# Kernel optimization log

Measured on AMD Instinct MI355X. Metric: run time of the kernel, lower is better.

Reference implementation:

```python
import jax, jax.numpy as jnp
import numpy as np

R = 15  # receptive-field rows (self.rfield)
_NAMES = ['1x', '2x', '3x', '4x', '1e', '2e', '3e', '4e', '5', '6', '7', '8', '9']
_CIN = [3, 64, 64, 64, 3, 64, 64, 64, 64, 64, 64, 64, 64]
_COUT = [64, 64, 64, 64, 64, 64, 64, 64, 64, 64, 64, 64, 3]


def _leaky(x):
    return jnp.where(x >= 0, x, 0.01 * x)  # nn.LeakyReLU default slope


def _conv(x, w, b, ph):
    # 3x3 conv, stride 1, padding (ph, 1) matching torch Conv2d padding=[ph, 1]
    y = jax.lax.conv_general_dilated(x, w, (1, 1), ((ph, ph), (1, 1)),
                                     dimension_numbers=('NCHW', 'OIHW', 'NCHW'))
    return y + b[None, :, None, None]


def setup_inputs():
    key = jax.random.key(0)
    ks = jax.random.split(key, len(_NAMES) + 1)
    inp = {'x': jax.random.normal(ks[0], (1, 3, 31, 256), jnp.float32)}
    for j, n in enumerate(_NAMES):
        std = np.float32((2.0 / (_CIN[j] * 9)) ** 0.5)  # He init for 3x3 conv
        inp['w' + n] = jax.random.normal(ks[j + 1], (_COUT[j], _CIN[j], 3, 3), jnp.float32) * std
        inp['b' + n] = jnp.zeros((_COUT[j],), jnp.float32)
    return inp


def _predict(s, e, p):
    # x-branch: 15 rows -> 9 rows (three H-valid convs)
    for n, ph in (('1x', 1), ('2x', 0), ('3x', 0), ('4x', 0)):
        s = _leaky(_conv(s, p['w' + n], p['b' + n], ph))
    # e-branch
    for n, ph in (('1e', 1), ('2e', 0), ('3e', 0), ('4e', 0)):
        e = _leaky(_conv(e, p['w' + n], p['b' + n], ph))
    B, C, Hs, W = s.shape  # C == 64 -> per-pixel 8x8 matrices; Hs == R - 6 == 9
    sr = jnp.transpose(s, (0, 2, 3, 1)).reshape(B, Hs, W, 8, 8)
    er = jnp.transpose(e, (0, 2, 3, 1)).reshape(B, Hs, W, 8, 8)
    pr = jnp.einsum('bhwij,bhwjk->bhwik', er, sr).reshape(B, Hs, W, 64)
    pr = jnp.transpose(pr, (0, 3, 1, 2))  # [B,64,9,W]
    # fuse stack: 9 rows -> 1 row, then 64 -> 3 channels
    for n, ph in (('5', 0), ('6', 0), ('7', 0), ('8', 0), ('9', 1)):
        pr = _leaky(_conv(pr, p['w' + n], p['b' + n], ph))
    return pr  # [B, 3, 1, W]


def _forward(x, p):
    B, C, H, W = x.shape

    def step(ebuf, i):
        # torch code sets error = x (alias), so slice_x and slice_e are the SAME mutated buffer
        sl = jax.lax.dynamic_slice(ebuf, (0, 0, i, 0), (B, C, R, W))
        pr = _predict(sl, sl, p)
        # act_row reads row ky of the (mutated) x, but row ky is overwritten only after this read,
        # so it still equals the original input row
        act = jax.lax.dynamic_slice(x, (0, 0, i + R, 0), (B, C, 1, W))
        ebuf = jax.lax.dynamic_update_slice(ebuf, act - pr, (0, 0, i + R, 0))
        return ebuf, pr

    ebuf, preds = jax.lax.scan(step, x, jnp.arange(H - R))
    pred = jnp.transpose(preds[:, :, :, 0, :], (1, 2, 0, 3))  # [S,B,C,1,W] -> [B,C,S,W]
    # 'truth' is read from the in-place-mutated x, i.e. the residual buffer, matching the torch aliasing bug/behavior
    truth = ebuf[:, :, R:, :]
    return pred, truth


def reference(x, w1x, b1x, w2x, b2x, w3x, b3x, w4x, b4x, w1e, b1e, w2e, b2e, w3e, b3e, w4e, b4e, w5, b5, w6, b6, w7, b7, w8, b8, w9, b9):
    p = dict(w1x=w1x, b1x=b1x, w2x=w2x, b2x=b2x, w3x=w3x, b3x=b3x, w4x=w4x, b4x=b4x,
             w1e=w1e, b1e=b1e, w2e=w2e, b2e=b2e, w3e=w3e, b3e=b3e, w4e=w4e, b4e=b4e,
             w5=w5, b5=b5, w6=w6, b6=b6, w7=w7, b7=b7, w8=w8, b8=b8, w9=w9, b9=b9)
    return _forward(x, p)
```

## Files before the change

### kernel.cpp

```cpp
#include <hip/hip_runtime.h>

#define LEAKY(v) ((v) >= 0.f ? (v) : 0.01f * (v))

__global__ __launch_bounds__(256, 2) void conv3Q(
    const float* __restrict__ ebuf, int i0,
    const float* __restrict__ w0, const float* __restrict__ b0,
    const float* __restrict__ w1, const float* __restrict__ b1,
    float* __restrict__ out)
{
    const int lane = threadIdx.x & 63;
    const int wv   = threadIdx.x >> 6;
    const int h  = blockIdx.y;
    const int cq = blockIdx.z & 3;
    const int z  = blockIdx.z >> 2;
    const int cout0 = __builtin_amdgcn_readfirstlane(cq * 16 + wv * 4);
    const float* W  = (z ? w1 : w0) + cout0 * 27;
    const float* Bv = z ? b1 : b0;

    float a[4][4] = {};
    #pragma unroll
    for (int kh = 0; kh < 3; ++kh) {
        const int r = h - 1 + kh;
        const bool valid = (r >= 0 && r < 15);
        const float msk = valid ? 1.f : 0.f;
        #pragma unroll
        for (int c = 0; c < 3; ++c) {
            const float* rr = ebuf + c * (31 * 256) + (i0 + (valid ? r : 0)) * 256 + lane * 4;
            float4 v = *(const float4*)rr;
            v.x *= msk; v.y *= msk; v.z *= msk; v.w *= msk;
            float wl = __shfl_up(v.w, 1);   if (lane == 0)  wl = 0.f;
            float wr = __shfl_down(v.x, 1); if (lane == 63) wr = 0.f;
            const float win[6] = {wl, v.x, v.y, v.z, v.w, wr};
            #pragma unroll
            for (int j = 0; j < 4; ++j) {
                const float* wj = W + j * 27 + c * 9 + kh * 3;
                #pragma unroll
                for (int cc = 0; cc < 4; ++cc)
                    a[j][cc] += wj[0] * win[cc] + wj[1] * win[cc + 1] + wj[2] * win[cc + 2];
            }
        }
    }
    float* o = out + (size_t)z * 245760 + h * 256 + lane * 4;
    #pragma unroll
    for (int j = 0; j < 4; ++j) {
        const float bb = Bv[cout0 + j];
        float4 r4;
        r4.x = LEAKY(a[j][0] + bb);
        r4.y = LEAKY(a[j][1] + bb);
        r4.z = LEAKY(a[j][2] + bb);
        r4.w = LEAKY(a[j][3] + bb);
        *(float4*)(o + (cout0 + j) * (15 * 256)) = r4;
    }
}

template<int HOUT, int INH, int NZ>
__global__ __launch_bounds__(256, 2) void convYQ(
    const float* __restrict__ in,
    const float* __restrict__ w0, const float* __restrict__ b0,
    const float* __restrict__ w1, const float* __restrict__ b1,
    float* __restrict__ out)
{
    const int lane = threadIdx.x;
    const int y    = threadIdx.y;
    const int h  = blockIdx.y;
    const int gz = blockIdx.z;
    const int z    = (NZ == 2) ? (gz >> 6) : 0;
    const int cout = (NZ == 2) ? (gz & 63) : gz;
    const float* W  = (z ? w1 : w0) + cout * 576 + y * 16 * 9;
    const float* Bv = z ? b1 : b0;
    const float* ib = in + (size_t)z * (64 * INH * 256)
                         + y * 16 * (INH * 256) + h * 256 + lane * 4;

    float acc[4] = {};

    #pragma unroll 4
    for (int c = 0; c < 16; ++c) {
        const float* r_ = ib + c * (INH * 256);
        #pragma unroll
        for (int kh = 0; kh < 3; ++kh) {
            float4 v = *(const float4*)(r_ + kh * 256);
            float wl = __shfl_up(v.w, 1);   if (lane == 0)  wl = 0.f;
            float wr = __shfl_down(v.x, 1); if (lane == 63) wr = 0.f;
            const float win[6] = {wl, v.x, v.y, v.z, v.w, wr};
            const float* wj = W + c * 9 + kh * 3;
            #pragma unroll
            for (int cc = 0; cc < 4; ++cc)
                acc[cc] += wj[0] * win[cc] + wj[1] * win[cc + 1] + wj[2] * win[cc + 2];
        }
    }

    __shared__ float red[4][256];
    *(float4*)&red[y][lane * 4] = *(float4*)acc;
    __syncthreads();

    const int col = y * 64 + lane;
    float v = Bv[cout] + red[0][col] + red[1][col] + red[2][col] + red[3][col];
    float* o = out + (size_t)z * (64 * HOUT * 256) + cout * (HOUT * 256) + h * 256;
    o[col] = LEAKY(v);
}

__global__ __launch_bounds__(256, 2) void mm88(const float* __restrict__ tw,
                                               float* __restrict__ p0)
{
    const int idx = blockIdx.x * 256 + threadIdx.x;
    const int i   = blockIdx.y;
    const float* s = tw;
    const float* e = tw + 64 * 9 * 256;
    float sv[64];
    #pragma unroll
    for (int c = 0; c < 64; ++c) sv[c] = s[c * (9 * 256) + idx];
    float ev[8];
    #pragma unroll
    for (int j = 0; j < 8; ++j) ev[j] = e[(i * 8 + j) * (9 * 256) + idx];
    #pragma unroll
    for (int k = 0; k < 8; ++k) {
        float acc = 0.f;
        #pragma unroll
        for (int j = 0; j < 8; ++j) acc += ev[j] * sv[j * 8 + k];
        p0[(i * 8 + k) * (9 * 256) + idx] = acc;
    }
}

__global__ void conv9up(const float* __restrict__ pin, const float* __restrict__ w9,
                        const float* __restrict__ b9, const float* __restrict__ x,
                        float* __restrict__ ebuf, float* __restrict__ preds, int i)
{
    const int wcol = threadIdx.x;
    const int yq   = threadIdx.y;
    const int c0   = yq * 16;
    const bool mL = (wcol > 0), mR = (wcol < 255);
    float a0 = 0.f, a1 = 0.f, a2 = 0.f;

    #pragma unroll 4
    for (int c = 0; c < 16; ++c) {
        const int cin = c0 + c;
        const float* r_ = pin + cin * 256;
        float vm = mL ? r_[wcol - 1] : 0.f;
        float v0 = r_[wcol];
        float vp = mR ? r_[wcol + 1] : 0.f;
        const float* wk0 = w9 + (0 * 64 + cin) * 9 + 3;
        const float* wk1 = w9 + (1 * 64 + cin) * 9 + 3;
        const float* wk2 = w9 + (2 * 64 + cin) * 9 + 3;
        a0 += vm * wk0[0] + v0 * wk0[1] + vp * wk0[2];
        a1 += vm * wk1[0] + v0 * wk1[1] + vp * wk1[2];
        a2 += vm * wk2[0] + v0 * wk2[1] + vp * wk2[2];
    }

    __shared__ float red[4][3][256];
    red[yq][0][wcol] = a0;
    red[yq][1][wcol] = a1;
    red[yq][2][wcol] = a2;
    __syncthreads();

    if (yq == 0) {
        #pragma unroll
        for (int j = 0; j < 3; ++j) {
            float v = b9[j] + red[0][j][wcol] + red[1][j][wcol]
                            + red[2][j][wcol] + red[3][j][wcol];
            v = LEAKY(v);
            preds[i * 768 + j * 256 + wcol] = v;
            ebuf[j * 31 * 256 + (15 + i) * 256 + wcol] =
                x[j * 31 * 256 + (15 + i) * 256 + wcol] - v;
        }
    }
}

__global__ void finalize(const float* __restrict__ preds, const float* __restrict__ ebuf,
                         float* __restrict__ o)
{
    const int idx = blockIdx.x * 256 + threadIdx.x;
    if (idx >= 24576) return;
    if (idx < 12288) {
        const int c = idx >> 12;
        const int t = (idx >> 8) & 15;
        const int w = idx & 255;
        o[idx] = preds[t * 768 + c * 256 + w];
    } else {
        const int j = idx - 12288;
        const int c = j >> 12;
        const int t = (j >> 8) & 15;
        const int w = j & 255;
        o[idx] = ebuf[c * 31 * 256 + (15 + t) * 256 + w];
    }
}

extern "C" void kernel_launch(void* const* d_in, const int* in_sizes, int n_in,
                              void* d_out, int out_size, void* d_ws, size_t ws_size,
                              hipStream_t stream)
{
    const float* x   = (const float*)d_in[0];
    const float* w1x = (const float*)d_in[1];  const float* b1x = (const float*)d_in[2];
    const float* w2x = (const float*)d_in[3];  const float* b2x = (const float*)d_in[4];
    const float* w3x = (const float*)d_in[5];  const float* b3x = (const float*)d_in[6];
    const float* w4x = (const float*)d_in[7];  const float* b4x = (const float*)d_in[8];
    const float* w1e = (const float*)d_in[9];  const float* b1e = (const float*)d_in[10];
    const float* w2e = (const float*)d_in[11]; const float* b2e = (const float*)d_in[12];
    const float* w3e = (const float*)d_in[13]; const float* b3e = (const float*)d_in[14];
    const float* w4e = (const float*)d_in[15]; const float* b4e = (const float*)d_in[16];
    const float* w5  = (const float*)d_in[17]; const float* b5  = (const float*)d_in[18];
    const float* w6  = (const float*)d_in[19]; const float* b6  = (const float*)d_in[20];
    const float* w7  = (const float*)d_in[21]; const float* b7  = (const float*)d_in[22];
    const float* w8  = (const float*)d_in[23]; const float* b8  = (const float*)d_in[24];
    const float* w9  = (const float*)d_in[25]; const float* b9  = (const float*)d_in[26];

    float* ws    = (float*)d_ws;
    float* ebuf  = ws;
    float* tA    = ebuf + 23808;
    float* tB    = tA + 491520;
    float* p0    = tB + 491520;
    float* p1    = p0 + 147456;
    float* preds = p1 + 147456;

    hipMemcpyAsync(ebuf, x, 23808 * sizeof(float), hipMemcpyDeviceToDevice, stream);

    const dim3 cb(64, 4);
    for (int i = 0; i < 16; ++i) {
        conv3Q<<<dim3(1, 15, 8), 256, 0, stream>>>(ebuf, i, w1x, b1x, w1e, b1e, tA);
        convYQ<13, 15, 2><<<dim3(1, 13, 128), cb, 0, stream>>>(tA, w2x, b2x, w2e, b2e, tB);
        convYQ<11, 13, 2><<<dim3(1, 11, 128), cb, 0, stream>>>(tB, w3x, b3x, w3e, b3e, tA);
        convYQ<9, 11, 2><<<dim3(1, 9, 128), cb, 0, stream>>>(tA, w4x, b4x, w4e, b4e, tB);
        mm88<<<dim3(9, 8), 256, 0, stream>>>(tB, p0);
        convYQ<7, 9, 1><<<dim3(1, 7, 64), cb, 0, stream>>>(p0, w5, b5, w5, b5, p1);
        convYQ<5, 7, 1><<<dim3(1, 5, 64), cb, 0, stream>>>(p1, w6, b6, w6, b6, p0);
        convYQ<3, 5, 1><<<dim3(1, 3, 64), cb, 0, stream>>>(p0, w7, b7, w7, b7, p1);
        convYQ<1, 3, 1><<<dim3(1, 1, 64), cb, 0, stream>>>(p1, w8, b8, w8, b8, p0);
        conv9up<<<dim3(1, 1, 1), dim3(256, 4), 0, stream>>>(p0, w9, b9, x, ebuf, preds, i);
    }

    finalize<<<96, 256, 0, stream>>>(preds, ebuf, (float*)d_out);
}
```

Before: 1.919 ms.

## Recompute only changed rows per scan step using ring-buffered layer activations

Per-layer activations now live in ring buffers, with separate slots for the padded top and bottom rows. After the first full pass, each step recomputes only the rows that depend on the newly written error row or the shifted window, instead of redoing every layer over all rows. This removes most of the redundant conv work across the 16 sequential steps. In exchange the slot indexing is intricate and easy to get wrong, and each step still issues a similar number of small kernel launches.

```diff
diff --git a/kernel.cpp b/kernel.cpp
--- a/kernel.cpp
+++ b/kernel.cpp
@@ -2,10 +2,109 @@
 
 #define LEAKY(v) ((v) >= 0.f ? (v) : 0.01f * (v))
 
-__global__ __launch_bounds__(256, 2) void conv3Q(
-    const float* __restrict__ ebuf, int i0,
-    const float* __restrict__ w0, const float* __restrict__ b0,
-    const float* __restrict__ w1, const float* __restrict__ b1,
+#define CS   4608
+#define ZS1  294912
+#define TSL  16
+#define BSL  17
+#define EBCS 7936
+
+struct JobD { const float* t0; const float* t1; const float* t2; float* o; };
+struct IncP { JobD jd[6]; };
+
+__global__ __launch_bounds__(256, 2) void convInc(
+    IncP P, const float* __restrict__ W0, const float* __restrict__ B0,
+    const float* __restrict__ W1, const float* __restrict__ B1,
+    int zsel, int ics, int ocs)
+{
+    const int lane = threadIdx.x;
+    const int y    = threadIdx.y;
+    const int q    = blockIdx.x >> 6;
+    const int cout = blockIdx.x & 63;
+    const int z    = (zsel >> q) & 1;
+    const float* W  = (z ? W1 : W0) + cout * 576 + y * 144;
+    const float* Bv = z ? B1 : B0;
+    const JobD jd  = P.jd[q];
+    const int yo   = y * 16 * ics + lane * 4;
+    const float* t0 = jd.t0 + yo;
+    const float* t1 = jd.t1 + yo;
+    const float* t2 = jd.t2 + yo;
+
+    float acc[4] = {};
+    #pragma unroll 4
+    for (int c = 0; c < 16; ++c) {
+        #pragma unroll
+        for (int t = 0; t < 3; ++t) {
+            const float* rp = (t == 0 ? t0 : (t == 1 ? t1 : t2)) + c * ics;
+            float4 v = *(const float4*)rp;
+            float wl = __shfl_up(v.w, 1);   if (lane == 0)  wl = 0.f;
+            float wr = __shfl_down(v.x, 1); if (lane == 63) wr = 0.f;
+            const float win[6] = {wl, v.x, v.y, v.z, v.w, wr};
+            const float* wj = W + c * 9 + t * 3;
+            #pragma unroll
+            for (int cc = 0; cc < 4; ++cc)
+                acc[cc] += wj[0] * win[cc] + wj[1] * win[cc + 1] + wj[2] * win[cc + 2];
+        }
+    }
+
+    __shared__ float red[4][256];
+    *(float4*)&red[y][lane * 4] = *(float4*)acc;
+    __syncthreads();
+    const int col = y * 64 + lane;
+    float v = Bv[cout] + red[0][col] + red[1][col] + red[2][col] + red[3][col];
+    jd.o[cout * ocs + col] = LEAKY(v);
+}
+
+struct C3P { const float* t[3][3]; float* o[3][2]; };
+
+__global__ __launch_bounds__(256, 2) void conv3inc(
+    C3P P, const float* __restrict__ W0, const float* __restrict__ B0,
+    const float* __restrict__ W1, const float* __restrict__ B1)
+{
+    const int lane = threadIdx.x & 63;
+    const int wv   = threadIdx.x >> 6;
+    const int job  = blockIdx.x >> 3;
+    const int cq   = blockIdx.x & 3;
+    const int z    = (blockIdx.x >> 2) & 1;
+    const int cout0 = __builtin_amdgcn_readfirstlane(cq * 16 + wv * 4);
+    const float* W  = (z ? W1 : W0) + cout0 * 27;
+    const float* Bv = z ? B1 : B0;
+
+    float a[4][4] = {};
+    #pragma unroll
+    for (int t = 0; t < 3; ++t) {
+        const float* rp = P.t[job][t];
+        if (rp) {
+            #pragma unroll
+            for (int c = 0; c < 3; ++c) {
+                float4 v = *(const float4*)(rp + c * EBCS + lane * 4);
+                float wl = __shfl_up(v.w, 1);   if (lane == 0)  wl = 0.f;
+                float wr = __shfl_down(v.x, 1); if (lane == 63) wr = 0.f;
+                const float win[6] = {wl, v.x, v.y, v.z, v.w, wr};
+                #pragma unroll
+                for (int j = 0; j < 4; ++j) {
+                    const float* wj = W + j * 27 + c * 9 + t * 3;
+                    #pragma unroll
+                    for (int cc = 0; cc < 4; ++cc)
+                        a[j][cc] += wj[0] * win[cc] + wj[1] * win[cc + 1] + wj[2] * win[cc + 2];
+                }
+            }
+        }
+    }
+    float* o = P.o[job][z];
+    #pragma unroll
+    for (int j = 0; j < 4; ++j) {
+        const float bb = Bv[cout0 + j];
+        float4 r4;
+        r4.x = LEAKY(a[j][0] + bb); r4.y = LEAKY(a[j][1] + bb);
+        r4.z = LEAKY(a[j][2] + bb); r4.w = LEAKY(a[j][3] + bb);
+        *(float4*)(o + (cout0 + j) * CS + lane * 4) = r4;
+    }
+}
+
+__global__ __launch_bounds__(256, 2) void conv3B(
+    const float* __restrict__ ebuf,
+    const float* __restrict__ W0, const float* __restrict__ B0,
+    const float* __restrict__ W1, const float* __restrict__ B1,
     float* __restrict__ out)
 {
     const int lane = threadIdx.x & 63;
@@ -14,8 +113,8 @@
     const int cq = blockIdx.z & 3;
     const int z  = blockIdx.z >> 2;
     const int cout0 = __builtin_amdgcn_readfirstlane(cq * 16 + wv * 4);
-    const float* W  = (z ? w1 : w0) + cout0 * 27;
-    const float* Bv = z ? b1 : b0;
+    const float* W  = (z ? W1 : W0) + cout0 * 27;
+    const float* Bv = z ? B1 : B0;
 
     float a[4][4] = {};
     #pragma unroll
@@ -25,7 +124,7 @@
         const float msk = valid ? 1.f : 0.f;
         #pragma unroll
         for (int c = 0; c < 3; ++c) {
-            const float* rr = ebuf + c * (31 * 256) + (i0 + (valid ? r : 0)) * 256 + lane * 4;
+            const float* rr = ebuf + c * EBCS + (valid ? r : 0) * 256 + lane * 4;
             float4 v = *(const float4*)rr;
             v.x *= msk; v.y *= msk; v.z *= msk; v.w *= msk;
             float wl = __shfl_up(v.w, 1);   if (lane == 0)  wl = 0.f;
@@ -40,24 +139,23 @@
             }
         }
     }
-    float* o = out + (size_t)z * 245760 + h * 256 + lane * 4;
+    const int slot = (h == 0) ? TSL : (h == 14 ? BSL : (h & 15));
+    float* o = out + (size_t)z * ZS1 + slot * 256;
     #pragma unroll
     for (int j = 0; j < 4; ++j) {
         const float bb = Bv[cout0 + j];
         float4 r4;
-        r4.x = LEAKY(a[j][0] + bb);
-        r4.y = LEAKY(a[j][1] + bb);
-        r4.z = LEAKY(a[j][2] + bb);
-        r4.w = LEAKY(a[j][3] + bb);
-        *(float4*)(o + (cout0 + j) * (15 * 256)) = r4;
-    }
-}
-
-template<int HOUT, int INH, int NZ>
-__global__ __launch_bounds__(256, 2) void convYQ(
+        r4.x = LEAKY(a[j][0] + bb); r4.y = LEAKY(a[j][1] + bb);
+        r4.z = LEAKY(a[j][2] + bb); r4.w = LEAKY(a[j][3] + bb);
+        *(float4*)(o + (cout0 + j) * CS + lane * 4) = r4;
+    }
+}
+
+template<int HOUT, int HIN, int OFFI, int OFFO, int NZ>
+__global__ __launch_bounds__(256, 2) void convYB(
     const float* __restrict__ in,
-    const float* __restrict__ w0, const float* __restrict__ b0,
-    const float* __restrict__ w1, const float* __restrict__ b1,
+    const float* __restrict__ W0, const float* __restrict__ B0,
+    const float* __restrict__ W1, const float* __restrict__ B1,
     float* __restrict__ out)
 {
     const int lane = threadIdx.x;
@@ -66,23 +164,27 @@
     const int gz = blockIdx.z;
     const int z    = (NZ == 2) ? (gz >> 6) : 0;
     const int cout = (NZ == 2) ? (gz & 63) : gz;
-    const float* W  = (z ? w1 : w0) + cout * 576 + y * 16 * 9;
-    const float* Bv = z ? b1 : b0;
-    const float* ib = in + (size_t)z * (64 * INH * 256)
-                         + y * 16 * (INH * 256) + h * 256 + lane * 4;
+    const float* W  = (z ? W1 : W0) + cout * 576 + y * 144;
+    const float* Bv = z ? B1 : B0;
+    const float* ib = in + (size_t)z * ZS1 + y * 16 * CS + lane * 4;
+
+    int slot[3];
+    #pragma unroll
+    for (int t = 0; t < 3; ++t) {
+        const int g = h + t;
+        slot[t] = (g == 0) ? TSL : (g == HIN - 1 ? BSL : ((g + OFFI) & 15));
+    }
 
     float acc[4] = {};
-
     #pragma unroll 4
     for (int c = 0; c < 16; ++c) {
-        const float* r_ = ib + c * (INH * 256);
-        #pragma unroll
-        for (int kh = 0; kh < 3; ++kh) {
-            float4 v = *(const float4*)(r_ + kh * 256);
+        #pragma unroll
+        for (int t = 0; t < 3; ++t) {
+            float4 v = *(const float4*)(ib + c * CS + slot[t] * 256);
             float wl = __shfl_up(v.w, 1);   if (lane == 0)  wl = 0.f;
             float wr = __shfl_down(v.x, 1); if (lane == 63) wr = 0.f;
             const float win[6] = {wl, v.x, v.y, v.z, v.w, wr};
-            const float* wj = W + c * 9 + kh * 3;
+            const float* wj = W + c * 9 + t * 3;
             #pragma unroll
             for (int cc = 0; cc < 4; ++cc)
                 acc[cc] += wj[0] * win[cc] + wj[1] * win[cc + 1] + wj[2] * win[cc + 2];
@@ -92,32 +194,57 @@
     __shared__ float red[4][256];
     *(float4*)&red[y][lane * 4] = *(float4*)acc;
     __syncthreads();
-
     const int col = y * 64 + lane;
+    const int os = (h == 0) ? TSL : (h == HOUT - 1 ? BSL : ((h + OFFO) & 15));
     float v = Bv[cout] + red[0][col] + red[1][col] + red[2][col] + red[3][col];
-    float* o = out + (size_t)z * (64 * HOUT * 256) + cout * (HOUT * 256) + h * 256;
-    o[col] = LEAKY(v);
-}
-
-__global__ __launch_bounds__(256, 2) void mm88(const float* __restrict__ tw,
-                                               float* __restrict__ p0)
-{
-    const int idx = blockIdx.x * 256 + threadIdx.x;
-    const int i   = blockIdx.y;
-    const float* s = tw;
-    const float* e = tw + 64 * 9 * 256;
+    out[(size_t)z * ZS1 + cout * CS + os * 256 + col] = LEAKY(v);
+}
+
+__global__ __launch_bounds__(256, 2) void mmB(const float* __restrict__ L4R,
+                                              float* __restrict__ MMR)
+{
+    const int col = threadIdx.x;
+    const int r   = blockIdx.x;
+    const int ig  = blockIdx.y;
+    const int slot = (r == 0) ? TSL : (r == 8 ? BSL : ((r + 3) & 15));
+    const float* s = L4R + slot * 256 + col;
+    const float* e = L4R + ZS1 + slot * 256 + col;
     float sv[64];
     #pragma unroll
-    for (int c = 0; c < 64; ++c) sv[c] = s[c * (9 * 256) + idx];
+    for (int c = 0; c < 64; ++c) sv[c] = s[c * CS];
     float ev[8];
     #pragma unroll
-    for (int j = 0; j < 8; ++j) ev[j] = e[(i * 8 + j) * (9 * 256) + idx];
+    for (int j = 0; j < 8; ++j) ev[j] = e[(ig * 8 + j) * CS];
     #pragma unroll
     for (int k = 0; k < 8; ++k) {
         float acc = 0.f;
         #pragma unroll
         for (int j = 0; j < 8; ++j) acc += ev[j] * sv[j * 8 + k];
-        p0[(i * 8 + k) * (9 * 256) + idx] = acc;
+        MMR[(ig * 8 + k) * CS + slot * 256 + col] = acc;
+    }
+}
+
+struct MMP { const float* s[3]; const float* e[3]; float* o[3]; };
+__global__ __launch_bounds__(256, 2) void mminc(MMP P)
+{
+    const int col = threadIdx.x;
+    const int job = blockIdx.x;
+    const int ig  = blockIdx.y;
+    const float* s = P.s[job] + col;
+    const float* e = P.e[job] + col;
+    float sv[64];
+    #pragma unroll
+    for (int c = 0; c < 64; ++c) sv[c] = s[c * CS];
+    float ev[8];
+    #pragma unroll
+    for (int j = 0; j < 8; ++j) ev[j] = e[(ig * 8 + j) * CS];
+    float* o = P.o[job];
+    #pragma unroll
+    for (int k = 0; k < 8; ++k) {
+        float acc = 0.f;
+        #pragma unroll
+        for (int j = 0; j < 8; ++j) acc += ev[j] * sv[j * 8 + k];
+        o[(ig * 8 + k) * CS + col] = acc;
     }
 }
 
@@ -159,8 +286,8 @@
                             + red[2][j][wcol] + red[3][j][wcol];
             v = LEAKY(v);
             preds[i * 768 + j * 256 + wcol] = v;
-            ebuf[j * 31 * 256 + (15 + i) * 256 + wcol] =
-                x[j * 31 * 256 + (15 + i) * 256 + wcol] - v;
+            ebuf[j * EBCS + (15 + i) * 256 + wcol] =
+                x[j * EBCS + (15 + i) * 256 + wcol] - v;
         }
     }
 }
@@ -180,7 +307,7 @@
         const int c = j >> 12;
         const int t = (j >> 8) & 15;
         const int w = j & 255;
-        o[idx] = ebuf[c * 31 * 256 + (15 + t) * 256 + w];
+        o[idx] = ebuf[c * EBCS + (15 + t) * 256 + w];
     }
 }
 
@@ -205,26 +332,100 @@
 
     float* ws    = (float*)d_ws;
     float* ebuf  = ws;
-    float* tA    = ebuf + 23808;
-    float* tB    = tA + 491520;
-    float* p0    = tB + 491520;
-    float* p1    = p0 + 147456;
-    float* preds = p1 + 147456;
+    float* L1R   = ebuf + 23808;
+    float* L2R   = L1R + 589824;
+    float* L3R   = L2R + 589824;
+    float* L4R   = L3R + 589824;
+    float* MMR   = L4R + 589824;
+    float* L5R   = MMR + 294912;
+    float* L6R   = L5R + 294912;
+    float* L7b   = L6R + 294912;
+    float* L8b   = L7b + 49152;
+    float* preds = L8b + 16384;
+
+    auto S2 = [](int c) { return c & 15; };
+    auto r2 = [](float* b, int z, int slot) { return b + (size_t)z * ZS1 + slot * 256; };
+    auto r1 = [](float* b, int slot) { return b + slot * 256; };
 
     hipMemcpyAsync(ebuf, x, 23808 * sizeof(float), hipMemcpyDeviceToDevice, stream);
 
     const dim3 cb(64, 4);
+
+    conv3B<<<dim3(1, 15, 8), 256, 0, stream>>>(ebuf, w1x, b1x, w1e, b1e, L1R);
+    convYB<13, 15, 0, 1, 2><<<dim3(1, 13, 128), cb, 0, stream>>>(L1R, w2x, b2x, w2e, b2e, L2R);
+    convYB<11, 13, 1, 2, 2><<<dim3(1, 11, 128), cb, 0, stream>>>(L2R, w3x, b3x, w3e, b3e, L3R);
+    convYB<9, 11, 2, 3, 2><<<dim3(1, 9, 128), cb, 0, stream>>>(L3R, w4x, b4x, w4e, b4e, L4R);
+    mmB<<<dim3(9, 8), 256, 0, stream>>>(L4R, MMR);
+    convYB<7, 9, 3, 4, 1><<<dim3(1, 7, 64), cb, 0, stream>>>(MMR, w5, b5, w5, b5, L5R);
+    convYB<5, 7, 4, 5, 1><<<dim3(1, 5, 64), cb, 0, stream>>>(L5R, w6, b6, w6, b6, L6R);
+
     for (int i = 0; i < 16; ++i) {
-        conv3Q<<<dim3(1, 15, 8), 256, 0, stream>>>(ebuf, i, w1x, b1x, w1e, b1e, tA);
-        convYQ<13, 15, 2><<<dim3(1, 13, 128), cb, 0, stream>>>(tA, w2x, b2x, w2e, b2e, tB);
-        convYQ<11, 13, 2><<<dim3(1, 11, 128), cb, 0, stream>>>(tB, w3x, b3x, w3e, b3e, tA);
-        convYQ<9, 11, 2><<<dim3(1, 9, 128), cb, 0, stream>>>(tA, w4x, b4x, w4e, b4e, tB);
-        mm88<<<dim3(9, 8), 256, 0, stream>>>(tB, p0);
-        convYQ<7, 9, 1><<<dim3(1, 7, 64), cb, 0, stream>>>(p0, w5, b5, w5, b5, p1);
-        convYQ<5, 7, 1><<<dim3(1, 5, 64), cb, 0, stream>>>(p1, w6, b6, w6, b6, p0);
-        convYQ<3, 5, 1><<<dim3(1, 3, 64), cb, 0, stream>>>(p0, w7, b7, w7, b7, p1);
-        convYQ<1, 3, 1><<<dim3(1, 1, 64), cb, 0, stream>>>(p1, w8, b8, w8, b8, p0);
-        conv9up<<<dim3(1, 1, 1), dim3(256, 4), 0, stream>>>(p0, w9, b9, x, ebuf, preds, i);
+        if (i > 0) {
+            C3P p3 = {};
+            p3.t[0][0] = nullptr;                p3.t[0][1] = ebuf + i * 256;        p3.t[0][2] = ebuf + (i + 1) * 256;
+            p3.t[1][0] = ebuf + (i + 13) * 256;  p3.t[1][1] = ebuf + (i + 14) * 256; p3.t[1][2] = nullptr;
+            p3.t[2][0] = ebuf + (i + 12) * 256;  p3.t[2][1] = ebuf + (i + 13) * 256; p3.t[2][2] = ebuf + (i + 14) * 256;
+            for (int z = 0; z < 2; ++z) {
+                p3.o[0][z] = r2(L1R, z, TSL);
+                p3.o[1][z] = r2(L1R, z, BSL);
+                p3.o[2][z] = r2(L1R, z, S2(i + 13));
+            }
+            conv3inc<<<24, 256, 0, stream>>>(p3, w1x, b1x, w1e, b1e);
+
+            IncP p2 = {};
+            for (int z = 0; z < 2; ++z) {
+                p2.jd[0 * 2 + z] = { r2(L1R, z, TSL),        r2(L1R, z, S2(i + 1)),  r2(L1R, z, S2(i + 2)),  r2(L2R, z, TSL) };
+                p2.jd[1 * 2 + z] = { r2(L1R, z, S2(i + 12)), r2(L1R, z, S2(i + 13)), r2(L1R, z, BSL),        r2(L2R, z, BSL) };
+                p2.jd[2 * 2 + z] = { r2(L1R, z, S2(i + 11)), r2(L1R, z, S2(i + 12)), r2(L1R, z, S2(i + 13)), r2(L2R, z, S2(i + 12)) };
+            }
+            convInc<<<384, cb, 0, stream>>>(p2, w2x, b2x, w2e, b2e, 42, CS, CS);
+
+            IncP p3i = {};
+            for (int z = 0; z < 2; ++z) {
+                p3i.jd[0 * 2 + z] = { r2(L2R, z, TSL),        r2(L2R, z, S2(i + 2)),  r2(L2R, z, S2(i + 3)),  r2(L3R, z, TSL) };
+                p3i.jd[1 * 2 + z] = { r2(L2R, z, S2(i + 11)), r2(L2R, z, S2(i + 12)), r2(L2R, z, BSL),        r2(L3R, z, BSL) };
+                p3i.jd[2 * 2 + z] = { r2(L2R, z, S2(i + 10)), r2(L2R, z, S2(i + 11)), r2(L2R, z, S2(i + 12)), r2(L3R, z, S2(i + 11)) };
+            }
+            convInc<<<384, cb, 0, stream>>>(p3i, w3x, b3x, w3e, b3e, 42, CS, CS);
+
+            IncP p4 = {};
+            for (int z = 0; z < 2; ++z) {
+                p4.jd[0 * 2 + z] = { r2(L3R, z, TSL),        r2(L3R, z, S2(i + 3)),  r2(L3R, z, S2(i + 4)),  r2(L4R, z, TSL) };
+                p4.jd[1 * 2 + z] = { r2(L3R, z, S2(i + 10)), r2(L3R, z, S2(i + 11)), r2(L3R, z, BSL),        r2(L4R, z, BSL) };
+                p4.jd[2 * 2 + z] = { r2(L3R, z, S2(i + 9)),  r2(L3R, z, S2(i + 10)), r2(L3R, z, S2(i + 11)), r2(L4R, z, S2(i + 10)) };
+            }
+            convInc<<<384, cb, 0, stream>>>(p4, w4x, b4x, w4e, b4e, 42, CS, CS);
+
+            MMP pm;
+            pm.s[0] = r2(L4R, 0, TSL);        pm.e[0] = r2(L4R, 1, TSL);        pm.o[0] = r1(MMR, TSL);
+            pm.s[1] = r2(L4R, 0, BSL);        pm.e[1] = r2(L4R, 1, BSL);        pm.o[1] = r1(MMR, BSL);
+            pm.s[2] = r2(L4R, 0, S2(i + 10)); pm.e[2] = r2(L4R, 1, S2(i + 10)); pm.o[2] = r1(MMR, S2(i + 10));
+            mminc<<<dim3(3, 8), 256, 0, stream>>>(pm);
+
+            IncP p5 = {};
+            p5.jd[0] = { r1(MMR, TSL),       r1(MMR, S2(i + 4)),  r1(MMR, S2(i + 5)),  r1(L5R, TSL) };
+            p5.jd[1] = { r1(MMR, S2(i + 9)), r1(MMR, S2(i + 10)), r1(MMR, BSL),        r1(L5R, BSL) };
+            p5.jd[2] = { r1(MMR, S2(i + 8)), r1(MMR, S2(i + 9)),  r1(MMR, S2(i + 10)), r1(L5R, S2(i + 9)) };
+            convInc<<<192, cb, 0, stream>>>(p5, w5, b5, w5, b5, 0, CS, CS);
+
+            IncP p6 = {};
+            p6.jd[0] = { r1(L5R, TSL),       r1(L5R, S2(i + 5)), r1(L5R, S2(i + 6)), r1(L6R, TSL) };
+            p6.jd[1] = { r1(L5R, S2(i + 8)), r1(L5R, S2(i + 9)), r1(L5R, BSL),       r1(L6R, BSL) };
+            p6.jd[2] = { r1(L5R, S2(i + 7)), r1(L5R, S2(i + 8)), r1(L5R, S2(i + 9)), r1(L6R, S2(i + 8)) };
+            convInc<<<192, cb, 0, stream>>>(p6, w6, b6, w6, b6, 0, CS, CS);
+        }
+
+        IncP p7 = {};
+        p7.jd[0] = { r1(L6R, TSL),       r1(L6R, S2(i + 6)), r1(L6R, S2(i + 7)), L7b };
+        p7.jd[1] = { r1(L6R, S2(i + 6)), r1(L6R, S2(i + 7)), r1(L6R, S2(i + 8)), L7b + 256 };
+        p7.jd[2] = { r1(L6R, S2(i + 7)), r1(L6R, S2(i + 8)), r1(L6R, BSL),       L7b + 512 };
+        convInc<<<192, cb, 0, stream>>>(p7, w7, b7, w7, b7, 0, CS, 768);
+
+        IncP p8 = {};
+        p8.jd[0] = { L7b, L7b + 256, L7b + 512, L8b };
+        convInc<<<64, cb, 0, stream>>>(p8, w8, b8, w8, b8, 0, 768, 256);
+
+        conv9up<<<dim3(1, 1, 1), dim3(256, 4), 0, stream>>>(L8b, w9, b9, x, ebuf, preds, i);
     }
 
     finalize<<<96, 256, 0, stream>>>(preds, ebuf, (float*)d_out);
```

Measured after the change: 1.905 ms. Within noise of the previous version (-0.7%).
